# Kernel optimization log

Measured on AMD Instinct MI355X. Metric: run time of the kernel, lower is better.

Reference implementation:

```python
import jax, jax.numpy as jnp
import numpy as np

B, N, C, H = 4, 1024, 1024, 16
D = C // H                      # head_dim = 64
FFH = int(int(C * 4.0) * 2 / 3) # 2730
EPS = 1e-6


def rmsnorm(x, w):
    return w * (x * jax.lax.rsqrt(jnp.mean(x * x, axis=-1, keepdims=True) + EPS))


def setup_inputs() -> dict:
    key = jax.random.key(0)
    ks = jax.random.split(key, 12)
    s = 0.02
    return {
        "x": jax.random.normal(ks[0], (B, N, C), jnp.float32),
        "c": jax.random.normal(ks[1], (B, C), jnp.float32),
        "norm1_w": jnp.ones((C,), jnp.float32),
        "norm2_w": jnp.ones((C,), jnp.float32),
        "qkv_w": jax.random.normal(ks[2], (3 * C, C), jnp.float32) * s,
        "qkv_b": jnp.zeros((3 * C,), jnp.float32),
        "q_norm_w": jnp.ones((D,), jnp.float32),
        "k_norm_w": jnp.ones((D,), jnp.float32),
        "proj_w": jax.random.normal(ks[3], (C, C), jnp.float32) * s,
        "proj_b": jnp.zeros((C,), jnp.float32),
        "w12_w": jax.random.normal(ks[4], (2 * FFH, C), jnp.float32) * s,
        "w12_b": jnp.zeros((2 * FFH,), jnp.float32),
        "w3_w": jax.random.normal(ks[5], (C, FFH), jnp.float32) * s,
        "w3_b": jnp.zeros((C,), jnp.float32),
        "ada_w": jax.random.normal(ks[6], (6 * C, C), jnp.float32) * s,
        "ada_b": jnp.zeros((6 * C,), jnp.float32),
    }


def modulate(x, shift, scale):
    return x * (1.0 + scale[:, None, :]) + shift[:, None, :]


def attention(x, qkv_w, qkv_b, q_norm_w, k_norm_w, proj_w, proj_b):
    qkv = x @ qkv_w.T + qkv_b                       # (B,N,3C)
    qkv = qkv.reshape(B, N, 3, H, D)
    q, k, v = qkv[:, :, 0], qkv[:, :, 1], qkv[:, :, 2]   # (B,N,H,D)
    q = jnp.transpose(q, (0, 2, 1, 3))              # (B,H,N,D)
    k = jnp.transpose(k, (0, 2, 1, 3))
    v = jnp.transpose(v, (0, 2, 1, 3))
    q = rmsnorm(q, q_norm_w)
    k = rmsnorm(k, k_norm_w)
    attn = jnp.einsum("bhnd,bhmd->bhnm", q, k) / jnp.sqrt(jnp.float32(D))
    attn = jax.nn.softmax(attn, axis=-1)
    out = jnp.einsum("bhnm,bhmd->bhnd", attn, v)
    out = jnp.transpose(out, (0, 2, 1, 3)).reshape(B, N, C)
    return out @ proj_w.T + proj_b


def swiglu(x, w12_w, w12_b, w3_w, w3_b):
    x12 = x @ w12_w.T + w12_b                       # (B,N,2*FFH)
    x1, x2 = x12[..., :FFH], x12[..., FFH:]
    h = jax.nn.silu(x1) * x2
    return h @ w3_w.T + w3_b


def reference(x, c, norm1_w, norm2_w, qkv_w, qkv_b, q_norm_w, k_norm_w,
              proj_w, proj_b, w12_w, w12_b, w3_w, w3_b, ada_w, ada_b):
    ada = jax.nn.silu(c) @ ada_w.T + ada_b          # (B,6C)
    s1, g1, b1, s2, g2, b2 = jnp.split(ada, 6, axis=-1)
    a = attention(modulate(rmsnorm(x, norm1_w), s1, g1),
                  qkv_w, qkv_b, q_norm_w, k_norm_w, proj_w, proj_b)
    x = x + b1[:, None, :] * a
    m = swiglu(modulate(rmsnorm(x, norm2_w), s2, g2), w12_w, w12_b, w3_w, w3_b)
    x = x + b2[:, None, :] * m
    return x
```

## Files before the change

### kernel.cpp

```cpp
#include <hip/hip_runtime.h>

typedef short s16x8 __attribute__((ext_vector_type(8)));
typedef short s16x4 __attribute__((ext_vector_type(4)));
typedef float f32x4 __attribute__((ext_vector_type(4)));

#define B_   4
#define N_   1024
#define C_   1024
#define H_   16
#define D_   64
#define FFH_ 2730
#define FFP_ 2752

__device__ __forceinline__ short f2bf(float f) {
  unsigned u = __float_as_uint(f);
  u += 0x7fff + ((u >> 16) & 1);
  return (short)(unsigned short)(u >> 16);
}
__device__ __forceinline__ float silu(float x) { return x / (1.f + __expf(-x)); }

__device__ __forceinline__ void gload16(const void* g, void* l) {
  __builtin_amdgcn_global_load_lds(
      (const __attribute__((address_space(1))) unsigned*)g,
      (__attribute__((address_space(3))) unsigned*)l, 16, 0, 0);
}

__global__ void cvt3(const float* __restrict__ s0, short* __restrict__ d0, const int n0,
                     const float* __restrict__ s1, short* __restrict__ d1, const int n1,
                     const float* __restrict__ s2, short* __restrict__ d2, const int n2) {
  const int tot = n0 + n1 + n2;
  for (int i = blockIdx.x * 256 + threadIdx.x; i < tot; i += gridDim.x * 256) {
    const float* s; short* d; int j = i;
    if (j < n0)            { s = s0; d = d0; }
    else if ((j -= n0) < n1) { s = s1; d = d1; }
    else                   { j -= n1; s = s2; d = d2; }
    const float4 v = ((const float4*)s)[j];
    s16x4 o;
    o[0] = f2bf(v.x); o[1] = f2bf(v.y); o[2] = f2bf(v.z); o[3] = f2bf(v.w);
    *(s16x4*)(d + (size_t)j * 4) = o;
  }
}

__global__ void cvt_w3(const float* __restrict__ s, short* __restrict__ d) {
  const int col = blockIdx.x * 256 + threadIdx.x;
  const int row = blockIdx.y;
  if (col < FFP_)
    d[(size_t)row * FFP_ + col] = (col < FFH_) ? f2bf(s[(size_t)row * FFH_ + col]) : (short)0;
}

__global__ void ada_gemm(const float* __restrict__ c, const float* __restrict__ aw,
                         const float* __restrict__ ab, float* __restrict__ ada) {
  const int j = blockIdx.x;
  const int l = threadIdx.x;
  float acc[4] = {0.f, 0.f, 0.f, 0.f};
  const float4* wr = (const float4*)(aw + (size_t)j * 1024);
  #pragma unroll
  for (int p = 0; p < 4; ++p) {
    const float4 wv = wr[p * 64 + l];
    #pragma unroll
    for (int b = 0; b < 4; ++b) {
      const float4 cv = ((const float4*)(c + b * 1024))[p * 64 + l];
      acc[b] += silu(cv.x) * wv.x + silu(cv.y) * wv.y + silu(cv.z) * wv.z + silu(cv.w) * wv.w;
    }
  }
  #pragma unroll
  for (int b = 0; b < 4; ++b) {
    float a = acc[b];
    #pragma unroll
    for (int m = 1; m < 64; m <<= 1) a += __shfl_xor(a, m);
    if (l == 0) ada[b * 6144 + j] = a + ab[j];
  }
}

__global__ void rmsmod(const float* __restrict__ x, const float* __restrict__ wn,
                       const float* __restrict__ ada, const int sOff, const int gOff,
                       short* __restrict__ out) {
  const int row = blockIdx.x;
  const int b = row >> 10;
  const int t = threadIdx.x;
  const float4 v = ((const float4*)(x + (size_t)row * 1024))[t];
  float ss = v.x * v.x + v.y * v.y + v.z * v.z + v.w * v.w;
  #pragma unroll
  for (int m = 1; m < 64; m <<= 1) ss += __shfl_xor(ss, m);
  __shared__ float red[4];
  if ((t & 63) == 0) red[t >> 6] = ss;
  __syncthreads();
  const float rs = rsqrtf((red[0] + red[1] + red[2] + red[3]) * (1.f / 1024.f) + 1e-6f);
  const int j = t * 4;
  const float* sp = ada + b * 6144 + sOff + j;
  const float* gp = ada + b * 6144 + gOff + j;
  s16x4 o;
  o[0] = f2bf(v.x * rs * wn[j + 0] * (1.f + gp[0]) + sp[0]);
  o[1] = f2bf(v.y * rs * wn[j + 1] * (1.f + gp[1]) + sp[1]);
  o[2] = f2bf(v.z * rs * wn[j + 2] * (1.f + gp[2]) + sp[2]);
  o[3] = f2bf(v.w * rs * wn[j + 3] * (1.f + gp[3]) + sp[3]);
  *(s16x4*)(out + (size_t)row * 1024 + j) = o;
}

template <int EPI, int NT>
__launch_bounds__(256, 2)
__global__ void gemm_bt(const short* __restrict__ A, const short* __restrict__ Bt,
                        const int K,
                        const float* __restrict__ bias,
                        const float* __restrict__ adav,
                        const float* __restrict__ resid,
                        float* __restrict__ outF,
                        short* __restrict__ qbO, short* __restrict__ kbO,
                        short* __restrict__ vrO,
                        const float* __restrict__ qnw, const float* __restrict__ knw) {
  constexpr int NF = NT / 32;
  constexpr int BRW = NT / 4;
  __shared__ short As[128 * 64];
  __shared__ short Bs[NT * 64];
  const int t = threadIdx.x;
  const int l = t & 63;
  const int w = t >> 6;
  const int wr = (w >> 1) * 64, wc = (w & 1) * (NT / 2);

  const int nwg = gridDim.x * gridDim.y;
  int lin = blockIdx.y * gridDim.x + blockIdx.x;
  lin = (lin & 7) * (nwg >> 3) + (lin >> 3);
  const int m0 = (lin / gridDim.x) * 128;
  const int n0 = (lin % gridDim.x) * NT;
  const int nT = K >> 6;

  f32x4 acc[4][NF];
  const f32x4 z4 = {0.f, 0.f, 0.f, 0.f};
  #pragma unroll
  for (int i = 0; i < 4; ++i)
    #pragma unroll
    for (int j = 0; j < NF; ++j) acc[i][j] = z4;

  const int lr = l >> 3;
  const int lc = (l & 7) ^ lr;
  const short* gAs = A + (size_t)(m0 + w * 32 + lr) * K + lc * 8;
  const short* gBs = Bt + (size_t)(n0 + w * BRW + lr) * K + lc * 8;
  short* lA = As + (w * 32) * 64;
  short* lB = Bs + (w * BRW) * 64;

  for (int kt = 0; kt < nT; ++kt) {
    if (kt) __syncthreads();
    const int ko = kt * 64;
    #pragma unroll
    for (int p = 0; p < 4; ++p)
      gload16(gAs + (size_t)p * 8 * K + ko, lA + p * 8 * 64);
    #pragma unroll
    for (int p = 0; p < NT / 32; ++p)
      gload16(gBs + (size_t)p * 8 * K + ko, lB + p * 8 * 64);
    __syncthreads();
    #pragma unroll
    for (int kk = 0; kk < 2; ++kk) {
      const int c16 = kk * 4 + (l >> 4);
      s16x8 af[4], bfr[NF];
      #pragma unroll
      for (int mf = 0; mf < 4; ++mf) {
        const int r = wr + mf * 16 + (l & 15);
        af[mf] = *(const s16x8*)&As[r * 64 + ((c16 ^ (r & 7)) << 3)];
      }
      #pragma unroll
      for (int nf = 0; nf < NF; ++nf) {
        const int r = wc + nf * 16 + (l & 15);
        bfr[nf] = *(const s16x8*)&Bs[r * 64 + ((c16 ^ (r & 7)) << 3)];
      }
      __builtin_amdgcn_s_setprio(1);
      #pragma unroll
      for (int mf = 0; mf < 4; ++mf)
        #pragma unroll
        for (int nf = 0; nf < NF; ++nf)
          acc[mf][nf] = __builtin_amdgcn_mfma_f32_16x16x32_bf16(af[mf], bfr[nf], acc[mf][nf], 0, 0, 0);
      __builtin_amdgcn_s_setprio(0);
    }
  }

  if (EPI == 1) {
    const int bIdx = m0 >> 10;
    #pragma unroll
    for (int mf = 0; mf < 4; ++mf) {
      const int row = m0 + wr + mf * 16 + ((l >> 4) << 2);
      #pragma unroll
      for (int nf = 0; nf < NF; ++nf) {
        const int col = n0 + wc + nf * 16 + (l & 15);
        const float bsv = bias[col];
        const float av = adav[bIdx * 6144 + col];
        #pragma unroll
        for (int i = 0; i < 4; ++i) {
          const float v = acc[mf][nf][i] + bsv;
          outF[(size_t)(row + i) * 1024 + col] =
              resid[(size_t)(row + i) * 1024 + col] + av * v;
        }
      }
    }
  }

  if (EPI == 2) {
    const int colB = n0 + wc;
    const int sec = colB >> 10;
    const int hh = (colB >> 6) & 15;
    if (sec < 2) {
      short* dst = sec ? kbO : qbO;
      const float* nw = sec ? knw : qnw;
      const float scl = sec ? 1.f : 0.125f;
      #pragma unroll
      for (int mf = 0; mf < 4; ++mf) {
        #pragma unroll
        for (int i = 0; i < 4; ++i) {
          const int row = m0 + wr + mf * 16 + ((l >> 4) << 2) + i;
          float vv[4];
          float ss = 0.f;
          #pragma unroll
          for (int nf = 0; nf < 4; ++nf) {
            vv[nf] = acc[mf][nf & (NF - 1)][i] + bias[colB + nf * 16 + (l & 15)];
            ss += vv[nf] * vv[nf];
          }
          ss += __shfl_xor(ss, 1); ss += __shfl_xor(ss, 2);
          ss += __shfl_xor(ss, 4); ss += __shfl_xor(ss, 8);
          const float rs = rsqrtf(ss * (1.f / 64.f) + 1e-6f) * scl;
          const int bb = row >> 10, nn = row & 1023;
          #pragma unroll
          for (int nf = 0; nf < 4; ++nf) {
            const int d = nf * 16 + (l & 15);
            dst[((size_t)(bb * 16 + hh) * 1024 + nn) * 64 + d] = f2bf(vv[nf] * rs * nw[d]);
          }
        }
      }
    } else {
      #pragma unroll
      for (int mf = 0; mf < 4; ++mf)
        #pragma unroll
        for (int nf = 0; nf < 4; ++nf) {
          const int col = colB + nf * 16 + (l & 15);
          const float bsv = bias[col];
          #pragma unroll
          for (int i = 0; i < 4; ++i) {
            const int row = m0 + wr + mf * 16 + ((l >> 4) << 2) + i;
            vrO[(size_t)row * 1024 + (col - 2048)] = f2bf(acc[mf][nf & (NF - 1)][i] + bsv);
          }
        }
    }
  }
}

__launch_bounds__(256, 2)
__global__ void gemm_w12(const short* __restrict__ A, const short* __restrict__ Bt,
                         const float* __restrict__ bias, short* __restrict__ outH) {
  __shared__ short As[128 * 64];
  __shared__ short B1s[128 * 64];
  __shared__ short B2s[128 * 64];
  const int t = threadIdx.x;
  const int l = t & 63;
  const int w = t >> 6;
  const int wr = (w >> 1) * 64, wc = (w & 1) * 64;

  const int nwg = gridDim.x * gridDim.y;
  int lin = blockIdx.y * gridDim.x + blockIdx.x;
  lin = (lin & 7) * (nwg >> 3) + (lin >> 3);
  const int m0 = (lin / gridDim.x) * 128;
  const int n0 = (lin % gridDim.x) * 128;

  f32x4 a1[4][4], a2[4][4];
  const f32x4 z4 = {0.f, 0.f, 0.f, 0.f};
  #pragma unroll
  for (int i = 0; i < 4; ++i)
    #pragma unroll
    for (int j = 0; j < 4; ++j) { a1[i][j] = z4; a2[i][j] = z4; }

  const int lr = l >> 3;
  const int lc = (l & 7) ^ lr;
  const short* gAs = A + (size_t)(m0 + w * 32 + lr) * 1024 + lc * 8;
  const int rbase = n0 + w * 32 + lr;
  short* lA = As + (w * 32) * 64;
  short* lB1 = B1s + (w * 32) * 64;
  short* lB2 = B2s + (w * 32) * 64;

  for (int kt = 0; kt < 16; ++kt) {
    if (kt) __syncthreads();
    const int ko = kt * 64;
    #pragma unroll
    for (int p = 0; p < 4; ++p) {
      int j = rbase + p * 8;
      if (j >= FFH_) j = FFH_ - 1;
      gload16(gAs + (size_t)p * 8 * 1024 + ko, lA + p * 8 * 64);
      gload16(Bt + (size_t)j * 1024 + ko + lc * 8, lB1 + p * 8 * 64);
      gload16(Bt + (size_t)(j + FFH_) * 1024 + ko + lc * 8, lB2 + p * 8 * 64);
    }
    __syncthreads();
    #pragma unroll
    for (int kk = 0; kk < 2; ++kk) {
      const int c16 = kk * 4 + (l >> 4);
      s16x8 af[4], b1f[4], b2f[4];
      #pragma unroll
      for (int mf = 0; mf < 4; ++mf) {
        const int r = wr + mf * 16 + (l & 15);
        af[mf] = *(const s16x8*)&As[r * 64 + ((c16 ^ (r & 7)) << 3)];
      }
      #pragma unroll
      for (int nf = 0; nf < 4; ++nf) {
        const int r = wc + nf * 16 + (l & 15);
        const int idx = r * 64 + ((c16 ^ (r & 7)) << 3);
        b1f[nf] = *(const s16x8*)&B1s[idx];
        b2f[nf] = *(const s16x8*)&B2s[idx];
      }
      __builtin_amdgcn_s_setprio(1);
      #pragma unroll
      for (int mf = 0; mf < 4; ++mf)
        #pragma unroll
        for (int nf = 0; nf < 4; ++nf) {
          a1[mf][nf] = __builtin_amdgcn_mfma_f32_16x16x32_bf16(af[mf], b1f[nf], a1[mf][nf], 0, 0, 0);
          a2[mf][nf] = __builtin_amdgcn_mfma_f32_16x16x32_bf16(af[mf], b2f[nf], a2[mf][nf], 0, 0, 0);
        }
      __builtin_amdgcn_s_setprio(0);
    }
  }

  #pragma unroll
  for (int mf = 0; mf < 4; ++mf) {
    const int row = m0 + wr + mf * 16 + ((l >> 4) << 2);
    #pragma unroll
    for (int nf = 0; nf < 4; ++nf) {
      const int col = n0 + wc + nf * 16 + (l & 15);
      if (col < FFP_) {
        const bool real = col < FFH_;
        const float bb1 = real ? bias[col] : 0.f;
        const float bb2 = real ? bias[col + FFH_] : 0.f;
        #pragma unroll
        for (int i = 0; i < 4; ++i) {
          float o = 0.f;
          if (real) {
            const float v1 = a1[mf][nf][i] + bb1;
            const float v2 = a2[mf][nf][i] + bb2;
            o = silu(v1) * v2;
          }
          outH[(size_t)(row + i) * FFP_ + col] = f2bf(o);
        }
      }
    }
  }
}

__global__ void v_trans(const short* __restrict__ vr, short* __restrict__ vt) {
  __shared__ short ld[64][72];
  const int t = threadIdx.x;
  const int bh = blockIdx.y, b = bh >> 4, h = bh & 15;
  const int n0 = blockIdx.x * 64;
  const int nl = t >> 2, cb = (t & 3) * 16;
  const short* src = vr + (size_t)(b * 1024 + n0 + nl) * 1024 + h * 64 + cb;
  *(s16x8*)&ld[nl][cb] = *(const s16x8*)src;
  *(s16x8*)&ld[nl][cb + 8] = *(const s16x8*)(src + 8);
  __syncthreads();
  const int d = t >> 2, np = (t & 3) * 16;
  short* dst = vt + (size_t)(bh * 64 + d) * 1024 + n0 + np;
  s16x8 o0, o1;
  #pragma unroll
  for (int p = 0; p < 8; ++p) { o0[p] = ld[np + p][d]; o1[p] = ld[np + 8 + p][d]; }
  *(s16x8*)dst = o0;
  *(s16x8*)(dst + 8) = o1;
}

__launch_bounds__(256, 2)
__global__ void attn(const short* __restrict__ qb, const short* __restrict__ kb,
                     const short* __restrict__ vt, short* __restrict__ ob) {
  __shared__ short Ks[64 * 64];
  __shared__ short Vs[64 * 64];
  __shared__ short Pl[4][32 * 64];
  const int t = threadIdx.x, l = t & 63, w = t >> 6;
  const int bh = blockIdx.y, b = bh >> 4, h = bh & 15;
  const int q0 = blockIdx.x * 128 + w * 32;
  const short* qp = qb + (size_t)bh * (N_ * D_);
  const short* kp = kb + (size_t)bh * (N_ * D_);
  const short* vp = vt + (size_t)bh * (D_ * N_);

  s16x8 qf[2][2];
  #pragma unroll
  for (int mf = 0; mf < 2; ++mf)
    #pragma unroll
    for (int kk = 0; kk < 2; ++kk)
      qf[mf][kk] = *(const s16x8*)&qp[(q0 + mf * 16 + (l & 15)) * 64 + kk * 32 + ((l >> 4) * 8)];

  f32x4 aco[2][4];
  float rm[2][4], rl[2][4];
  const f32x4 z4 = {0.f, 0.f, 0.f, 0.f};
  #pragma unroll
  for (int mf = 0; mf < 2; ++mf) {
    #pragma unroll
    for (int nd = 0; nd < 4; ++nd) aco[mf][nd] = z4;
    #pragma unroll
    for (int i = 0; i < 4; ++i) { rm[mf][i] = -1e30f; rl[mf][i] = 0.f; }
  }

  const int sr = t >> 2, sc = (t & 3) * 2;
  s16x8 rk[2], rv[2];
  #pragma unroll
  for (int p = 0; p < 2; ++p) {
    rk[p] = *(const s16x8*)&kp[sr * 64 + (sc + p) * 8];
    rv[p] = *(const s16x8*)&vp[sr * 1024 + (sc + p) * 8];
  }

  for (int kt = 0; kt < 16; ++kt) {
    if (kt) __syncthreads();
    #pragma unroll
    for (int p = 0; p < 2; ++p) {
      const int cs = ((sc + p) ^ (sr & 7)) << 3;
      *(s16x8*)&Ks[sr * 64 + cs] = rk[p];
      *(s16x8*)&Vs[sr * 64 + cs] = rv[p];
    }
    __syncthreads();
    if (kt < 15) {
      const int kv0 = (kt + 1) * 64;
      #pragma unroll
      for (int p = 0; p < 2; ++p) {
        rk[p] = *(const s16x8*)&kp[(kv0 + sr) * 64 + (sc + p) * 8];
        rv[p] = *(const s16x8*)&vp[sr * 1024 + kv0 + (sc + p) * 8];
      }
    }

    f32x4 s[2][4];
    #pragma unroll
    for (int mf = 0; mf < 2; ++mf)
      #pragma unroll
      for (int nf = 0; nf < 4; ++nf) s[mf][nf] = z4;

    #pragma unroll
    for (int kk = 0; kk < 2; ++kk) {
      const int c16 = kk * 4 + (l >> 4);
      s16x8 kf[4];
      #pragma unroll
      for (int nf = 0; nf < 4; ++nf) {
        const int r = nf * 16 + (l & 15);
        kf[nf] = *(const s16x8*)&Ks[r * 64 + ((c16 ^ (r & 7)) << 3)];
      }
      __builtin_amdgcn_s_setprio(1);
      #pragma unroll
      for (int mf = 0; mf < 2; ++mf)
        #pragma unroll
        for (int nf = 0; nf < 4; ++nf)
          s[mf][nf] = __builtin_amdgcn_mfma_f32_16x16x32_bf16(qf[mf][kk], kf[nf], s[mf][nf], 0, 0, 0);
      __builtin_amdgcn_s_setprio(0);
    }

    #pragma unroll
    for (int mf = 0; mf < 2; ++mf) {
      #pragma unroll
      for (int i = 0; i < 4; ++i) {
        float pm = fmaxf(fmaxf(s[mf][0][i], s[mf][1][i]), fmaxf(s[mf][2][i], s[mf][3][i]));
        pm = fmaxf(pm, __shfl_xor(pm, 1));
        pm = fmaxf(pm, __shfl_xor(pm, 2));
        pm = fmaxf(pm, __shfl_xor(pm, 4));
        pm = fmaxf(pm, __shfl_xor(pm, 8));
        const float nm = fmaxf(rm[mf][i], pm);
        const float corr = __expf(rm[mf][i] - nm);
        rm[mf][i] = nm;
        float rs = 0.f;
        #pragma unroll
        for (int nf = 0; nf < 4; ++nf) {
          const float p = __expf(s[mf][nf][i] - nm);
          s[mf][nf][i] = p;
          rs += p;
        }
        rs += __shfl_xor(rs, 1);
        rs += __shfl_xor(rs, 2);
        rs += __shfl_xor(rs, 4);
        rs += __shfl_xor(rs, 8);
        rl[mf][i] = rl[mf][i] * corr + rs;
        #pragma unroll
        for (int nd = 0; nd < 4; ++nd) aco[mf][nd][i] *= corr;
      }
    }

    short* pw = &Pl[w][0];
    #pragma unroll
    for (int mf = 0; mf < 2; ++mf)
      #pragma unroll
      for (int nf = 0; nf < 4; ++nf)
        #pragma unroll
        for (int i = 0; i < 4; ++i) {
          const int row = mf * 16 + ((l >> 4) << 2) + i;
          const int col = nf * 16 + (l & 15);
          pw[row * 64 + (((col >> 3) ^ (row & 7)) << 3) + (col & 7)] = f2bf(s[mf][nf][i]);
        }

    #pragma unroll
    for (int kk = 0; kk < 2; ++kk) {
      const int c16 = kk * 4 + (l >> 4);
      s16x8 vf[4];
      #pragma unroll
      for (int nd = 0; nd < 4; ++nd) {
        const int r = nd * 16 + (l & 15);
        vf[nd] = *(const s16x8*)&Vs[r * 64 + ((c16 ^ (r & 7)) << 3)];
      }
      __builtin_amdgcn_s_setprio(1);
      #pragma unroll
      for (int mf = 0; mf < 2; ++mf) {
        const int pr = mf * 16 + (l & 15);
        const s16x8 pf = *(const s16x8*)&pw[pr * 64 + ((c16 ^ (pr & 7)) << 3)];
        #pragma unroll
        for (int nd = 0; nd < 4; ++nd)
          aco[mf][nd] = __builtin_amdgcn_mfma_f32_16x16x32_bf16(pf, vf[nd], aco[mf][nd], 0, 0, 0);
      }
      __builtin_amdgcn_s_setprio(0);
    }
  }

  #pragma unroll
  for (int mf = 0; mf < 2; ++mf)
    #pragma unroll
    for (int i = 0; i < 4; ++i) {
      const float inv = 1.f / rl[mf][i];
      const int row = q0 + mf * 16 + ((l >> 4) << 2) + i;
      #pragma unroll
      for (int nd = 0; nd < 4; ++nd) {
        const int col = h * 64 + nd * 16 + (l & 15);
        ob[(size_t)(b * 1024 + row) * 1024 + col] = f2bf(aco[mf][nd][i] * inv);
      }
    }
}

extern "C" void kernel_launch(void* const* d_in, const int* in_sizes, int n_in,
                              void* d_out, int out_size, void* d_ws, size_t ws_size,
                              hipStream_t stream) {
  const float* x     = (const float*)d_in[0];
  const float* c     = (const float*)d_in[1];
  const float* n1w   = (const float*)d_in[2];
  const float* n2w   = (const float*)d_in[3];
  const float* qkvw  = (const float*)d_in[4];
  const float* qkvb  = (const float*)d_in[5];
  const float* qnw   = (const float*)d_in[6];
  const float* knw   = (const float*)d_in[7];
  const float* projw = (const float*)d_in[8];
  const float* projb = (const float*)d_in[9];
  const float* w12w  = (const float*)d_in[10];
  const float* w12b  = (const float*)d_in[11];
  const float* w3w   = (const float*)d_in[12];
  const float* w3b   = (const float*)d_in[13];
  const float* adaw  = (const float*)d_in[14];
  const float* adab  = (const float*)d_in[15];
  float* outp = (float*)d_out;

  char* ws = (char*)d_ws;
  size_t off = 0;
  auto alloc = [&](size_t bytes) { void* p = ws + off; off += (bytes + 255) & ~(size_t)255; return p; };
  short* WQKV = (short*)alloc(3072ull * 1024 * 2);
  short* WPROJ = (short*)alloc(1024ull * 1024 * 2);
  short* W12B = (short*)alloc(5460ull * 1024 * 2);
  short* W3B  = (short*)alloc(1024ull * FFP_ * 2);
  float* ADA  = (float*)alloc(4ull * 6144 * 4);
  short* H1   = (short*)alloc(4096ull * 1024 * 2);
  short* QBF  = (short*)alloc(64ull * 1024 * 64 * 2);
  short* KBF  = (short*)alloc(64ull * 1024 * 64 * 2);
  short* VROW = (short*)alloc(4096ull * 1024 * 2);
  short* VTB  = (short*)alloc(64ull * 64 * 1024 * 2);
  short* OBF  = (short*)alloc(4096ull * 1024 * 2);
  float* X1   = (float*)alloc(4096ull * 1024 * 4);
  short* H2   = (short*)alloc(4096ull * 1024 * 2);
  short* HB   = (short*)alloc(4096ull * FFP_ * 2);

  cvt3<<<2048, 256, 0, stream>>>(qkvw, WQKV, 3072 * 1024 / 4,
                                 projw, WPROJ, 1024 * 1024 / 4,
                                 w12w, W12B, 5460 * 1024 / 4);
  cvt_w3<<<dim3(11, 1024), 256, 0, stream>>>(w3w, W3B);
  ada_gemm<<<6144, 64, 0, stream>>>(c, adaw, adab, ADA);
  rmsmod<<<4096, 256, 0, stream>>>(x, n1w, ADA, 0, 1024, H1);
  gemm_bt<2, 128><<<dim3(24, 32), 256, 0, stream>>>(H1, WQKV, 1024, qkvb,
      nullptr, nullptr, nullptr, QBF, KBF, VROW, qnw, knw);
  v_trans<<<dim3(16, 64), 256, 0, stream>>>(VROW, VTB);
  attn<<<dim3(8, 64), 256, 0, stream>>>(QBF, KBF, VTB, OBF);
  gemm_bt<1, 64><<<dim3(16, 32), 256, 0, stream>>>(OBF, WPROJ, 1024, projb,
      ADA + 2048, x, X1, nullptr, nullptr, nullptr, nullptr, nullptr);
  rmsmod<<<4096, 256, 0, stream>>>(X1, n2w, ADA, 3072, 4096, H2);
  gemm_w12<<<dim3(22, 32), 256, 0, stream>>>(H2, W12B, w12b, HB);
  gemm_bt<1, 64><<<dim3(16, 32), 256, 0, stream>>>(HB, W3B, FFP_, w3b,
      ADA + 5120, X1, outp, nullptr, nullptr, nullptr, nullptr, nullptr);
}
```

Before: 271.9 us.

## Use 256-row tiles with 8 waves for QKV/W12 GEMMs and store residual in bf16

The QKV and W12 GEMMs now use 512-thread blocks with 256x128 output tiles, so each B tile loaded from global memory is reused across twice as many rows and half as many workgroups are launched. The intermediate residual X1 is stored in bf16 instead of fp32, and a new bf16-input rmsnorm/modulate kernel reads it, cutting residual traffic. In exchange the residual carries bf16 rounding error into the final output, and the larger tiles need more LDS and registers per block, which may lower occupancy.

```diff
diff --git a/kernel.cpp b/kernel.cpp
--- a/kernel.cpp
+++ b/kernel.cpp
@@ -16,6 +16,9 @@
   unsigned u = __float_as_uint(f);
   u += 0x7fff + ((u >> 16) & 1);
   return (short)(unsigned short)(u >> 16);
+}
+__device__ __forceinline__ float bf2f(short s) {
+  return __uint_as_float(((unsigned)(unsigned short)s) << 16);
 }
 __device__ __forceinline__ float silu(float x) { return x / (1.f + __expf(-x)); }
 
@@ -97,46 +100,183 @@
   *(s16x4*)(out + (size_t)row * 1024 + j) = o;
 }
 
-template <int EPI, int NT>
+__global__ void rmsmod_b(const short* __restrict__ x, const float* __restrict__ wn,
+                         const float* __restrict__ ada, const int sOff, const int gOff,
+                         short* __restrict__ out) {
+  const int row = blockIdx.x;
+  const int b = row >> 10;
+  const int t = threadIdx.x;
+  const s16x4 vb = *(const s16x4*)(x + (size_t)row * 1024 + t * 4);
+  const float v0 = bf2f(vb[0]), v1 = bf2f(vb[1]), v2 = bf2f(vb[2]), v3 = bf2f(vb[3]);
+  float ss = v0 * v0 + v1 * v1 + v2 * v2 + v3 * v3;
+  #pragma unroll
+  for (int m = 1; m < 64; m <<= 1) ss += __shfl_xor(ss, m);
+  __shared__ float red[4];
+  if ((t & 63) == 0) red[t >> 6] = ss;
+  __syncthreads();
+  const float rs = rsqrtf((red[0] + red[1] + red[2] + red[3]) * (1.f / 1024.f) + 1e-6f);
+  const int j = t * 4;
+  const float* sp = ada + b * 6144 + sOff + j;
+  const float* gp = ada + b * 6144 + gOff + j;
+  s16x4 o;
+  o[0] = f2bf(v0 * rs * wn[j + 0] * (1.f + gp[0]) + sp[0]);
+  o[1] = f2bf(v1 * rs * wn[j + 1] * (1.f + gp[1]) + sp[1]);
+  o[2] = f2bf(v2 * rs * wn[j + 2] * (1.f + gp[2]) + sp[2]);
+  o[3] = f2bf(v3 * rs * wn[j + 3] * (1.f + gp[3]) + sp[3]);
+  *(s16x4*)(out + (size_t)row * 1024 + j) = o;
+}
+
+__launch_bounds__(512, 4)
+__global__ void gemm_qkv(const short* __restrict__ A, const short* __restrict__ Bt,
+                         const float* __restrict__ bias,
+                         short* __restrict__ qbO, short* __restrict__ kbO,
+                         short* __restrict__ vrO,
+                         const float* __restrict__ qnw, const float* __restrict__ knw) {
+  __shared__ short As[256 * 64];
+  __shared__ short Bs[128 * 64];
+  const int t = threadIdx.x;
+  const int l = t & 63;
+  const int w = t >> 6;
+  const int wr = (w >> 1) * 64;
+  const int wc = (w & 1) * 64;
+  const int K = 1024;
+
+  const int nwg = gridDim.x * gridDim.y;
+  int lin = blockIdx.y * gridDim.x + blockIdx.x;
+  lin = (lin & 7) * (nwg >> 3) + (lin >> 3);
+  const int m0 = (lin / gridDim.x) * 256;
+  const int n0 = (lin % gridDim.x) * 128;
+
+  f32x4 acc[4][4];
+  const f32x4 z4 = {0.f, 0.f, 0.f, 0.f};
+  #pragma unroll
+  for (int i = 0; i < 4; ++i)
+    #pragma unroll
+    for (int j = 0; j < 4; ++j) acc[i][j] = z4;
+
+  const int lr = l >> 3;
+  const int lc = (l & 7) ^ lr;
+  const short* gAs = A + (size_t)(m0 + w * 32 + lr) * K + lc * 8;
+  const short* gBs = Bt + (size_t)(n0 + w * 16 + lr) * K + lc * 8;
+  short* lA = As + (w * 32) * 64;
+  short* lB = Bs + (w * 16) * 64;
+
+  for (int kt = 0; kt < 16; ++kt) {
+    if (kt) __syncthreads();
+    const int ko = kt * 64;
+    #pragma unroll
+    for (int p = 0; p < 4; ++p)
+      gload16(gAs + (size_t)p * 8 * K + ko, lA + p * 8 * 64);
+    #pragma unroll
+    for (int p = 0; p < 2; ++p)
+      gload16(gBs + (size_t)p * 8 * K + ko, lB + p * 8 * 64);
+    __syncthreads();
+    #pragma unroll
+    for (int kk = 0; kk < 2; ++kk) {
+      const int c16 = kk * 4 + (l >> 4);
+      s16x8 af[4], bfr[4];
+      #pragma unroll
+      for (int mf = 0; mf < 4; ++mf) {
+        const int r = wr + mf * 16 + (l & 15);
+        af[mf] = *(const s16x8*)&As[r * 64 + ((c16 ^ (r & 7)) << 3)];
+      }
+      #pragma unroll
+      for (int nf = 0; nf < 4; ++nf) {
+        const int r = wc + nf * 16 + (l & 15);
+        bfr[nf] = *(const s16x8*)&Bs[r * 64 + ((c16 ^ (r & 7)) << 3)];
+      }
+      __builtin_amdgcn_s_setprio(1);
+      #pragma unroll
+      for (int mf = 0; mf < 4; ++mf)
+        #pragma unroll
+        for (int nf = 0; nf < 4; ++nf)
+          acc[mf][nf] = __builtin_amdgcn_mfma_f32_16x16x32_bf16(af[mf], bfr[nf], acc[mf][nf], 0, 0, 0);
+      __builtin_amdgcn_s_setprio(0);
+    }
+  }
+
+  const int colB = n0 + wc;
+  const int sec = colB >> 10;
+  const int hh = (colB >> 6) & 15;
+  if (sec < 2) {
+    short* dst = sec ? kbO : qbO;
+    const float* nw = sec ? knw : qnw;
+    const float scl = sec ? 1.f : 0.125f;
+    #pragma unroll
+    for (int mf = 0; mf < 4; ++mf) {
+      #pragma unroll
+      for (int i = 0; i < 4; ++i) {
+        const int row = m0 + wr + mf * 16 + ((l >> 4) << 2) + i;
+        float vv[4];
+        float ss = 0.f;
+        #pragma unroll
+        for (int nf = 0; nf < 4; ++nf) {
+          vv[nf] = acc[mf][nf][i] + bias[colB + nf * 16 + (l & 15)];
+          ss += vv[nf] * vv[nf];
+        }
+        ss += __shfl_xor(ss, 1); ss += __shfl_xor(ss, 2);
+        ss += __shfl_xor(ss, 4); ss += __shfl_xor(ss, 8);
+        const float rs = rsqrtf(ss * (1.f / 64.f) + 1e-6f) * scl;
+        const int bb = row >> 10, nn = row & 1023;
+        #pragma unroll
+        for (int nf = 0; nf < 4; ++nf) {
+          const int d = nf * 16 + (l & 15);
+          dst[((size_t)(bb * 16 + hh) * 1024 + nn) * 64 + d] = f2bf(vv[nf] * rs * nw[d]);
+        }
+      }
+    }
+  } else {
+    #pragma unroll
+    for (int mf = 0; mf < 4; ++mf)
+      #pragma unroll
+      for (int nf = 0; nf < 4; ++nf) {
+        const int col = colB + nf * 16 + (l & 15);
+        const float bsv = bias[col];
+        #pragma unroll
+        for (int i = 0; i < 4; ++i) {
+          const int row = m0 + wr + mf * 16 + ((l >> 4) << 2) + i;
+          vrO[(size_t)row * 1024 + (col - 2048)] = f2bf(acc[mf][nf][i] + bsv);
+        }
+      }
+  }
+}
+
+template <int MODE>
 __launch_bounds__(256, 2)
-__global__ void gemm_bt(const short* __restrict__ A, const short* __restrict__ Bt,
+__global__ void gemm_pw(const short* __restrict__ A, const short* __restrict__ Bt,
                         const int K,
                         const float* __restrict__ bias,
                         const float* __restrict__ adav,
-                        const float* __restrict__ resid,
-                        float* __restrict__ outF,
-                        short* __restrict__ qbO, short* __restrict__ kbO,
-                        short* __restrict__ vrO,
-                        const float* __restrict__ qnw, const float* __restrict__ knw) {
-  constexpr int NF = NT / 32;
-  constexpr int BRW = NT / 4;
+                        const float* __restrict__ residF,
+                        const short* __restrict__ residB,
+                        void* __restrict__ outP) {
   __shared__ short As[128 * 64];
-  __shared__ short Bs[NT * 64];
+  __shared__ short Bs[64 * 64];
   const int t = threadIdx.x;
   const int l = t & 63;
   const int w = t >> 6;
-  const int wr = (w >> 1) * 64, wc = (w & 1) * (NT / 2);
+  const int wr = (w >> 1) * 64, wc = (w & 1) * 32;
 
   const int nwg = gridDim.x * gridDim.y;
   int lin = blockIdx.y * gridDim.x + blockIdx.x;
   lin = (lin & 7) * (nwg >> 3) + (lin >> 3);
   const int m0 = (lin / gridDim.x) * 128;
-  const int n0 = (lin % gridDim.x) * NT;
+  const int n0 = (lin % gridDim.x) * 64;
   const int nT = K >> 6;
 
-  f32x4 acc[4][NF];
+  f32x4 acc[4][2];
   const f32x4 z4 = {0.f, 0.f, 0.f, 0.f};
   #pragma unroll
   for (int i = 0; i < 4; ++i)
     #pragma unroll
-    for (int j = 0; j < NF; ++j) acc[i][j] = z4;
+    for (int j = 0; j < 2; ++j) acc[i][j] = z4;
 
   const int lr = l >> 3;
   const int lc = (l & 7) ^ lr;
   const short* gAs = A + (size_t)(m0 + w * 32 + lr) * K + lc * 8;
-  const short* gBs = Bt + (size_t)(n0 + w * BRW + lr) * K + lc * 8;
+  const short* gBs = Bt + (size_t)(n0 + w * 16 + lr) * K + lc * 8;
   short* lA = As + (w * 32) * 64;
-  short* lB = Bs + (w * BRW) * 64;
+  short* lB = Bs + (w * 16) * 64;
 
   for (int kt = 0; kt < nT; ++kt) {
     if (kt) __syncthreads();
@@ -145,20 +285,20 @@
     for (int p = 0; p < 4; ++p)
       gload16(gAs + (size_t)p * 8 * K + ko, lA + p * 8 * 64);
     #pragma unroll
-    for (int p = 0; p < NT / 32; ++p)
+    for (int p = 0; p < 2; ++p)
       gload16(gBs + (size_t)p * 8 * K + ko, lB + p * 8 * 64);
     __syncthreads();
     #pragma unroll
     for (int kk = 0; kk < 2; ++kk) {
       const int c16 = kk * 4 + (l >> 4);
-      s16x8 af[4], bfr[NF];
+      s16x8 af[4], bfr[2];
       #pragma unroll
       for (int mf = 0; mf < 4; ++mf) {
         const int r = wr + mf * 16 + (l & 15);
         af[mf] = *(const s16x8*)&As[r * 64 + ((c16 ^ (r & 7)) << 3)];
       }
       #pragma unroll
-      for (int nf = 0; nf < NF; ++nf) {
+      for (int nf = 0; nf < 2; ++nf) {
         const int r = wc + nf * 16 + (l & 15);
         bfr[nf] = *(const s16x8*)&Bs[r * 64 + ((c16 ^ (r & 7)) << 3)];
       }
@@ -166,95 +306,50 @@
       #pragma unroll
       for (int mf = 0; mf < 4; ++mf)
         #pragma unroll
-        for (int nf = 0; nf < NF; ++nf)
+        for (int nf = 0; nf < 2; ++nf)
           acc[mf][nf] = __builtin_amdgcn_mfma_f32_16x16x32_bf16(af[mf], bfr[nf], acc[mf][nf], 0, 0, 0);
       __builtin_amdgcn_s_setprio(0);
     }
   }
 
-  if (EPI == 1) {
-    const int bIdx = m0 >> 10;
-    #pragma unroll
-    for (int mf = 0; mf < 4; ++mf) {
-      const int row = m0 + wr + mf * 16 + ((l >> 4) << 2);
-      #pragma unroll
-      for (int nf = 0; nf < NF; ++nf) {
-        const int col = n0 + wc + nf * 16 + (l & 15);
-        const float bsv = bias[col];
-        const float av = adav[bIdx * 6144 + col];
-        #pragma unroll
-        for (int i = 0; i < 4; ++i) {
-          const float v = acc[mf][nf][i] + bsv;
-          outF[(size_t)(row + i) * 1024 + col] =
-              resid[(size_t)(row + i) * 1024 + col] + av * v;
-        }
-      }
-    }
-  }
-
-  if (EPI == 2) {
-    const int colB = n0 + wc;
-    const int sec = colB >> 10;
-    const int hh = (colB >> 6) & 15;
-    if (sec < 2) {
-      short* dst = sec ? kbO : qbO;
-      const float* nw = sec ? knw : qnw;
-      const float scl = sec ? 1.f : 0.125f;
-      #pragma unroll
-      for (int mf = 0; mf < 4; ++mf) {
-        #pragma unroll
-        for (int i = 0; i < 4; ++i) {
-          const int row = m0 + wr + mf * 16 + ((l >> 4) << 2) + i;
-          float vv[4];
-          float ss = 0.f;
-          #pragma unroll
-          for (int nf = 0; nf < 4; ++nf) {
-            vv[nf] = acc[mf][nf & (NF - 1)][i] + bias[colB + nf * 16 + (l & 15)];
-            ss += vv[nf] * vv[nf];
-          }
-          ss += __shfl_xor(ss, 1); ss += __shfl_xor(ss, 2);
-          ss += __shfl_xor(ss, 4); ss += __shfl_xor(ss, 8);
-          const float rs = rsqrtf(ss * (1.f / 64.f) + 1e-6f) * scl;
-          const int bb = row >> 10, nn = row & 1023;
-          #pragma unroll
-          for (int nf = 0; nf < 4; ++nf) {
-            const int d = nf * 16 + (l & 15);
-            dst[((size_t)(bb * 16 + hh) * 1024 + nn) * 64 + d] = f2bf(vv[nf] * rs * nw[d]);
-          }
-        }
-      }
-    } else {
-      #pragma unroll
-      for (int mf = 0; mf < 4; ++mf)
-        #pragma unroll
-        for (int nf = 0; nf < 4; ++nf) {
-          const int col = colB + nf * 16 + (l & 15);
-          const float bsv = bias[col];
-          #pragma unroll
-          for (int i = 0; i < 4; ++i) {
-            const int row = m0 + wr + mf * 16 + ((l >> 4) << 2) + i;
-            vrO[(size_t)row * 1024 + (col - 2048)] = f2bf(acc[mf][nf & (NF - 1)][i] + bsv);
-          }
-        }
-    }
-  }
-}
-
-__launch_bounds__(256, 2)
+  const int bIdx = m0 >> 10;
+  #pragma unroll
+  for (int mf = 0; mf < 4; ++mf) {
+    const int row = m0 + wr + mf * 16 + ((l >> 4) << 2);
+    #pragma unroll
+    for (int nf = 0; nf < 2; ++nf) {
+      const int col = n0 + wc + nf * 16 + (l & 15);
+      const float bsv = bias[col];
+      const float av = adav[bIdx * 6144 + col];
+      #pragma unroll
+      for (int i = 0; i < 4; ++i) {
+        const float v = acc[mf][nf][i] + bsv;
+        const size_t idx = (size_t)(row + i) * 1024 + col;
+        if (MODE == 1)
+          ((short*)outP)[idx] = f2bf(residF[idx] + av * v);
+        else
+          ((float*)outP)[idx] = bf2f(residB[idx]) + av * v;
+      }
+    }
+  }
+}
+
+__launch_bounds__(512, 4)
 __global__ void gemm_w12(const short* __restrict__ A, const short* __restrict__ Bt,
                          const float* __restrict__ bias, short* __restrict__ outH) {
-  __shared__ short As[128 * 64];
+  __shared__ short As[256 * 64];
   __shared__ short B1s[128 * 64];
   __shared__ short B2s[128 * 64];
   const int t = threadIdx.x;
   const int l = t & 63;
   const int w = t >> 6;
-  const int wr = (w >> 1) * 64, wc = (w & 1) * 64;
+  const int wr = (w >> 1) * 64;
+  const int wc = (w & 1) * 64;
 
   const int nwg = gridDim.x * gridDim.y;
   int lin = blockIdx.y * gridDim.x + blockIdx.x;
   lin = (lin & 7) * (nwg >> 3) + (lin >> 3);
-  const int m0 = (lin / gridDim.x) * 128;
+  const int m0 = (lin / gridDim.x) * 256;
   const int n0 = (lin % gridDim.x) * 128;
 
   f32x4 a1[4][4], a2[4][4];
@@ -267,19 +362,21 @@
   const int lr = l >> 3;
   const int lc = (l & 7) ^ lr;
   const short* gAs = A + (size_t)(m0 + w * 32 + lr) * 1024 + lc * 8;
-  const int rbase = n0 + w * 32 + lr;
+  const int rbase = n0 + w * 16 + lr;
   short* lA = As + (w * 32) * 64;
-  short* lB1 = B1s + (w * 32) * 64;
-  short* lB2 = B2s + (w * 32) * 64;
+  short* lB1 = B1s + (w * 16) * 64;
+  short* lB2 = B2s + (w * 16) * 64;
 
   for (int kt = 0; kt < 16; ++kt) {
     if (kt) __syncthreads();
     const int ko = kt * 64;
     #pragma unroll
-    for (int p = 0; p < 4; ++p) {
+    for (int p = 0; p < 4; ++p)
+      gload16(gAs + (size_t)p * 8 * 1024 + ko, lA + p * 8 * 64);
+    #pragma unroll
+    for (int p = 0; p < 2; ++p) {
       int j = rbase + p * 8;
       if (j >= FFH_) j = FFH_ - 1;
-      gload16(gAs + (size_t)p * 8 * 1024 + ko, lA + p * 8 * 64);
       gload16(Bt + (size_t)j * 1024 + ko + lc * 8, lB1 + p * 8 * 64);
       gload16(Bt + (size_t)(j + FFH_) * 1024 + ko + lc * 8, lB2 + p * 8 * 64);
     }
@@ -549,7 +646,7 @@
   short* VROW = (short*)alloc(4096ull * 1024 * 2);
   short* VTB  = (short*)alloc(64ull * 64 * 1024 * 2);
   short* OBF  = (short*)alloc(4096ull * 1024 * 2);
-  float* X1   = (float*)alloc(4096ull * 1024 * 4);
+  short* X1B  = (short*)alloc(4096ull * 1024 * 2);
   short* H2   = (short*)alloc(4096ull * 1024 * 2);
   short* HB   = (short*)alloc(4096ull * FFP_ * 2);
 
@@ -559,14 +656,13 @@
   cvt_w3<<<dim3(11, 1024), 256, 0, stream>>>(w3w, W3B);
   ada_gemm<<<6144, 64, 0, stream>>>(c, adaw, adab, ADA);
   rmsmod<<<4096, 256, 0, stream>>>(x, n1w, ADA, 0, 1024, H1);
-  gemm_bt<2, 128><<<dim3(24, 32), 256, 0, stream>>>(H1, WQKV, 1024, qkvb,
-      nullptr, nullptr, nullptr, QBF, KBF, VROW, qnw, knw);
+  gemm_qkv<<<dim3(24, 16), 512, 0, stream>>>(H1, WQKV, qkvb, QBF, KBF, VROW, qnw, knw);
   v_trans<<<dim3(16, 64), 256, 0, stream>>>(VROW, VTB);
   attn<<<dim3(8, 64), 256, 0, stream>>>(QBF, KBF, VTB, OBF);
-  gemm_bt<1, 64><<<dim3(16, 32), 256, 0, stream>>>(OBF, WPROJ, 1024, projb,
-      ADA + 2048, x, X1, nullptr, nullptr, nullptr, nullptr, nullptr);
-  rmsmod<<<4096, 256, 0, stream>>>(X1, n2w, ADA, 3072, 4096, H2);
-  gemm_w12<<<dim3(22, 32), 256, 0, stream>>>(H2, W12B, w12b, HB);
-  gemm_bt<1, 64><<<dim3(16, 32), 256, 0, stream>>>(HB, W3B, FFP_, w3b,
-      ADA + 5120, X1, outp, nullptr, nullptr, nullptr, nullptr, nullptr);
-}
+  gemm_pw<1><<<dim3(16, 32), 256, 0, stream>>>(OBF, WPROJ, 1024, projb,
+      ADA + 2048, x, nullptr, X1B);
+  rmsmod_b<<<4096, 256, 0, stream>>>(X1B, n2w, ADA, 3072, 4096, H2);
+  gemm_w12<<<dim3(22, 16), 512, 0, stream>>>(H2, W12B, w12b, HB);
+  gemm_pw<4><<<dim3(16, 32), 256, 0, stream>>>(HB, W3B, FFP_, w3b,
+      ADA + 5120, nullptr, X1B, outp);
+}
```

Result: slower. 798.7 us (+193.8%).
